# Performance work log

Measured on AMD Instinct MI355X. Metric: run time of the kernel, lower is better.

The kernel has to match this reference:

```python
import jax, jax.numpy as jnp
import numpy as np

D_MODEL = 1024
NUM_HEADS = 16
D_K = D_MODEL // NUM_HEADS
D_FF = 4096
THETA = 10000.0
EPS = 1e-5


def rmsnorm(x, w):
    ms = jnp.mean(jnp.square(x), axis=-1, keepdims=True)
    return x * jax.lax.rsqrt(ms + EPS) * w


def rope(x, pos):
    # x: [B, H, S, d_k]; pos: [S]
    half = x.shape[-1] // 2
    inv_freq = THETA ** (-jnp.arange(half, dtype=x.dtype) * 2.0 / x.shape[-1])  # [half]
    ang = pos.astype(x.dtype)[:, None] * inv_freq[None, :]  # [S, half]
    cos, sin = jnp.cos(ang), jnp.sin(ang)
    xe, xo = x[..., 0::2], x[..., 1::2]
    oe = xe * cos - xo * sin
    oo = xe * sin + xo * cos
    return jnp.stack([oe, oo], axis=-1).reshape(x.shape)


def setup_inputs() -> dict:
    key = jax.random.key(0)
    ks = jax.random.split(key, 10)
    std_d = 1.0 / np.sqrt(D_MODEL)
    std_f = 1.0 / np.sqrt(D_FF)
    B, S = 4, 2048
    return {
        "x": jax.random.normal(ks[0], (B, S, D_MODEL), dtype=jnp.float32),
        "token_positions": jnp.arange(S, dtype=jnp.int32),
        "q_proj": jax.random.normal(ks[1], (D_MODEL, D_MODEL), dtype=jnp.float32) * std_d,
        "k_proj": jax.random.normal(ks[2], (D_MODEL, D_MODEL), dtype=jnp.float32) * std_d,
        "v_proj": jax.random.normal(ks[3], (D_MODEL, D_MODEL), dtype=jnp.float32) * std_d,
        "o_proj": jax.random.normal(ks[4], (D_MODEL, D_MODEL), dtype=jnp.float32) * std_d,
        "w1": jax.random.normal(ks[5], (D_FF, D_MODEL), dtype=jnp.float32) * std_d,
        "w2": jax.random.normal(ks[6], (D_MODEL, D_FF), dtype=jnp.float32) * std_f,
        "w3": jax.random.normal(ks[7], (D_FF, D_MODEL), dtype=jnp.float32) * std_d,
        "ln1_w": jnp.ones((D_MODEL,), dtype=jnp.float32),
        "ln2_w": jnp.ones((D_MODEL,), dtype=jnp.float32),
    }


def reference(x, token_positions, q_proj, k_proj, v_proj, o_proj, w1, w2, w3, ln1_w, ln2_w):
    B, S, _ = x.shape
    x_ln = rmsnorm(x, ln1_w)
    q = x_ln @ q_proj.T
    k = x_ln @ k_proj.T
    v = x_ln @ v_proj.T
    # [B, S, D] -> [B, H, S, d_k]
    def split_heads(t):
        return t.reshape(B, S, NUM_HEADS, D_K).transpose(0, 2, 1, 3)
    q, k, v = split_heads(q), split_heads(k), split_heads(v)
    q = rope(q, token_positions)
    k = rope(k, token_positions)
    scores = jnp.einsum("bhqd,bhkd->bhqk", q, k) / jnp.sqrt(jnp.asarray(D_K, x.dtype))
    causal = jnp.tril(jnp.ones((S, S), dtype=bool))
    scores = jnp.where(causal, scores, -jnp.inf)
    attn = jax.nn.softmax(scores, axis=-1)
    out = jnp.einsum("bhqk,bhkd->bhqd", attn, v)
    out = out.transpose(0, 2, 1, 3).reshape(B, S, D_MODEL)
    x = x + out @ o_proj.T
    x_ln2 = rmsnorm(x, ln2_w)
    u = x_ln2 @ w1.T
    vff = x_ln2 @ w3.T
    ff = (u * jax.nn.sigmoid(u)) * vff
    return x + ff @ w2.T
```

## Files before the change

kernel.cpp:

```cpp
#include <hip/hip_runtime.h>
#include <hip/hip_bf16.h>


typedef unsigned short u16;
typedef __attribute__((ext_vector_type(8))) short short8;
typedef __attribute__((ext_vector_type(4))) float f32x4;
typedef __attribute__((ext_vector_type(16))) float f32x16;

#define MFMA16(a, b, c) __builtin_amdgcn_mfma_f32_16x16x32_bf16(a, b, c, 0, 0, 0)
#define MFMA32(a, b, c) __builtin_amdgcn_mfma_f32_32x32x16_bf16(a, b, c, 0, 0, 0)

__device__ __forceinline__ u16 f2b(float f) {
  union { float f; unsigned u; } x; x.f = f;
  unsigned r = x.u + 0x7FFFu + ((x.u >> 16) & 1u);
  return (u16)(r >> 16);
}
__device__ __forceinline__ float b2f(u16 h) {
  union { unsigned u; float f; } x; x.u = ((unsigned)h) << 16;
  return x.f;
}
__device__ __forceinline__ unsigned pkbf(float a, float b) {
  __hip_bfloat162 h = __float22bfloat162_rn(make_float2(a, b));
  union { __hip_bfloat162 h; unsigned u; } cv; cv.h = h;
  return cv.u;
}
__device__ __forceinline__ void async16(const void* g, void* l) {
  __builtin_amdgcn_global_load_lds(
      (const __attribute__((address_space(1))) void*)g,
      (__attribute__((address_space(3))) void*)l, 16, 0, 0);
}

template <int MODE>
__global__ __launch_bounds__(256, 2) void gemm_bt(
    const u16* __restrict__ A, const u16* __restrict__ B,
    u16* __restrict__ Cb, float* __restrict__ Cf, const float* __restrict__ R,
    int M, int N, int K) {
  __shared__ __align__(16) u16 As[128 * 64];
  __shared__ __align__(16) u16 Bs[128 * 64];
  const int tid = threadIdx.x;
  const int l = tid & 63, w = tid >> 6;
  const int wr = w & 1, wc = w >> 1;
  const int lr = l & 31, lh = l >> 5;
  const size_t m0 = (size_t)blockIdx.y * 128, n0 = (size_t)blockIdx.x * 128;
  f32x16 acc[2][2] = {};
  for (int k0 = 0; k0 < K; k0 += 64) {
#pragma unroll
    for (int t = 0; t < 4; ++t) {
      int c = t * 256 + tid;
      int r = c >> 3;
      int gc = ((c & 7) ^ (r & 7)) << 3;
      async16(A + (m0 + r) * (size_t)K + k0 + gc, &As[c * 8]);
    }
#pragma unroll
    for (int t = 0; t < 4; ++t) {
      int c = t * 256 + tid;
      int r = c >> 3;
      int gc = ((c & 7) ^ (r & 7)) << 3;
      async16(B + (n0 + r) * (size_t)K + k0 + gc, &Bs[c * 8]);
    }
    __syncthreads();
#pragma unroll
    for (int c = 0; c < 4; ++c) {
      const int c8 = c * 2 + lh;
      short8 af[2], bfr[2];
#pragma unroll
      for (int mi = 0; mi < 2; ++mi) {
        int r = wr * 64 + mi * 32 + lr;
        af[mi] = *(const short8*)&As[r * 64 + ((c8 ^ (r & 7)) << 3)];
      }
#pragma unroll
      for (int ni = 0; ni < 2; ++ni) {
        int r = wc * 64 + ni * 32 + lr;
        bfr[ni] = *(const short8*)&Bs[r * 64 + ((c8 ^ (r & 7)) << 3)];
      }
#pragma unroll
      for (int mi = 0; mi < 2; ++mi)
#pragma unroll
        for (int ni = 0; ni < 2; ++ni)
          acc[mi][ni] = MFMA32(af[mi], bfr[ni], acc[mi][ni]);
    }
    __syncthreads();
  }
#pragma unroll
  for (int mi = 0; mi < 2; ++mi)
#pragma unroll
    for (int ni = 0; ni < 2; ++ni) {
      size_t n = n0 + wc * 64 + ni * 32 + lr;
#pragma unroll
      for (int reg = 0; reg < 16; ++reg) {
        size_t m = m0 + wr * 64 + mi * 32 + (reg & 3) + 8 * (reg >> 2) + 4 * lh;
        float v = acc[mi][ni][reg];
        if (MODE == 0)
          Cb[m * (size_t)N + n] = f2b(v);
        else
          Cf[m * (size_t)N + n] = v + R[m * (size_t)N + n];
      }
    }
}

__global__ __launch_bounds__(256, 2) void ffn_gemm(
    const u16* __restrict__ A, const u16* __restrict__ B1,
    const u16* __restrict__ B3, u16* __restrict__ Hout, int M, int N, int K) {
  __shared__ __align__(16) u16 As[128 * 64];
  __shared__ __align__(16) u16 B1s[128 * 64];
  __shared__ __align__(16) u16 B3s[128 * 64];
  const int tid = threadIdx.x;
  const int l = tid & 63, w = tid >> 6;
  const int wr = w & 1, wc = w >> 1;
  const int lr = l & 31, lh = l >> 5;
  const size_t m0 = (size_t)blockIdx.y * 128, n0 = (size_t)blockIdx.x * 128;
  f32x16 a1[2][2] = {}, a3[2][2] = {};
  for (int k0 = 0; k0 < K; k0 += 64) {
#pragma unroll
    for (int t = 0; t < 4; ++t) {
      int c = t * 256 + tid;
      int r = c >> 3;
      int gc = ((c & 7) ^ (r & 7)) << 3;
      async16(A + (m0 + r) * (size_t)K + k0 + gc, &As[c * 8]);
      async16(B1 + (n0 + r) * (size_t)K + k0 + gc, &B1s[c * 8]);
      async16(B3 + (n0 + r) * (size_t)K + k0 + gc, &B3s[c * 8]);
    }
    __syncthreads();
#pragma unroll
    for (int c = 0; c < 4; ++c) {
      const int c8 = c * 2 + lh;
      short8 af[2], b1f[2], b3f[2];
#pragma unroll
      for (int mi = 0; mi < 2; ++mi) {
        int r = wr * 64 + mi * 32 + lr;
        af[mi] = *(const short8*)&As[r * 64 + ((c8 ^ (r & 7)) << 3)];
      }
#pragma unroll
      for (int ni = 0; ni < 2; ++ni) {
        int r = wc * 64 + ni * 32 + lr;
        b1f[ni] = *(const short8*)&B1s[r * 64 + ((c8 ^ (r & 7)) << 3)];
        b3f[ni] = *(const short8*)&B3s[r * 64 + ((c8 ^ (r & 7)) << 3)];
      }
#pragma unroll
      for (int mi = 0; mi < 2; ++mi)
#pragma unroll
        for (int ni = 0; ni < 2; ++ni) {
          a1[mi][ni] = MFMA32(af[mi], b1f[ni], a1[mi][ni]);
          a3[mi][ni] = MFMA32(af[mi], b3f[ni], a3[mi][ni]);
        }
    }
    __syncthreads();
  }
#pragma unroll
  for (int mi = 0; mi < 2; ++mi)
#pragma unroll
    for (int ni = 0; ni < 2; ++ni) {
      size_t n = n0 + wc * 64 + ni * 32 + lr;
#pragma unroll
      for (int reg = 0; reg < 16; ++reg) {
        size_t m = m0 + wr * 64 + mi * 32 + (reg & 3) + 8 * (reg >> 2) + 4 * lh;
        float u = a1[mi][ni][reg];
        float g = u / (1.0f + __expf(-u));
        Hout[m * (size_t)N + n] = f2b(g * a3[mi][ni][reg]);
      }
    }
}

__global__ __launch_bounds__(256, 2) void attn_k(
    const u16* __restrict__ qh, const u16* __restrict__ kh,
    const u16* __restrict__ vt, u16* __restrict__ aout) {
  __shared__ __align__(16) u16 Ks[128 * 64];
  __shared__ __align__(16) u16 Vs[64 * 128];
  __shared__ __align__(16) u16 Ps[64 * 136];
  const int tid = threadIdx.x;
  const int l = tid & 63, w = tid >> 6;
  const int q = l & 15, lq = l >> 4;
  const int q0 = (int)(gridDim.x - 1 - blockIdx.x) * 64;
  const int bh = blockIdx.y;
  const size_t base = (size_t)bh * (2048 * 64);
  const int nt = (q0 + 64 + 127) >> 7;
  const int qcol = q0 + w * 16 + q;

  short8 bq[2];
#pragma unroll
  for (int kk = 0; kk < 2; ++kk)
    bq[kk] = *(const short8*)(qh + base + (size_t)qcol * 64 + kk * 32 + lq * 8);

  f32x4 o[4] = {};
  float mI = -1e30f, lI = 0.0f;

  for (int it = 0; it < nt; ++it) {
    const int kv0 = it << 7;
    if (it) __syncthreads();
#pragma unroll
    for (int t = 0; t < 4; ++t) {
      int p = t * 256 + tid;
      int r = p >> 3, cs = p & 7;
      async16(kh + base + (size_t)(kv0 + r) * 64 + ((cs ^ (r & 7)) << 3), &Ks[p * 8]);
    }
#pragma unroll
    for (int t = 0; t < 4; ++t) {
      int p = t * 256 + tid;
      int r = p >> 4, cs = p & 15;
      async16(vt + base + (size_t)r * 2048 + kv0 + ((cs ^ (r & 15)) << 3), &Vs[p * 8]);
    }
    __syncthreads();
    f32x4 s[8] = {};
#pragma unroll
    for (int kk = 0; kk < 2; ++kk) {
#pragma unroll
      for (int mt = 0; mt < 8; ++mt) {
        int row = mt * 16 + q;
        short8 ak = *(const short8*)&Ks[row * 64 + (((kk * 4 + lq) ^ (q & 7)) << 3)];
        s[mt] = MFMA16(ak, bq[kk], s[mt]);
      }
    }
    if (it == nt - 1) {
#pragma unroll
      for (int mt = 0; mt < 8; ++mt)
#pragma unroll
        for (int r = 0; r < 4; ++r)
          if (kv0 + mt * 16 + lq * 4 + r > qcol) s[mt][r] = -1e30f;
    }
    float mx = -1e30f;
#pragma unroll
    for (int mt = 0; mt < 8; ++mt)
#pragma unroll
      for (int r = 0; r < 4; ++r) mx = fmaxf(mx, s[mt][r]);
    mx = fmaxf(mx, __shfl_xor(mx, 16, 64));
    mx = fmaxf(mx, __shfl_xor(mx, 32, 64));
    const float mn = fmaxf(mI, mx);
    const float al = exp2f(mI - mn);
    mI = mn;
    float rs = 0.0f;
#pragma unroll
    for (int mt = 0; mt < 8; ++mt)
#pragma unroll
      for (int r = 0; r < 4; ++r) {
        float p = exp2f(s[mt][r] - mn);
        s[mt][r] = p;
        rs += p;
      }
    rs += __shfl_xor(rs, 16, 64);
    rs += __shfl_xor(rs, 32, 64);
    lI = lI * al + rs;
#pragma unroll
    for (int mt = 0; mt < 4; ++mt)
#pragma unroll
      for (int r = 0; r < 4; ++r) o[mt][r] *= al;
    u16* pr = &Ps[(w * 16 + q) * 136];
#pragma unroll
    for (int mt = 0; mt < 8; ++mt) {
      uint2 pd;
      pd.x = pkbf(s[mt][0], s[mt][1]);
      pd.y = pkbf(s[mt][2], s[mt][3]);
      *(uint2*)&pr[mt * 16 + lq * 4] = pd;
    }
#pragma unroll
    for (int kk = 0; kk < 4; ++kk) {
      short8 bp = *(const short8*)&pr[kk * 32 + lq * 8];
#pragma unroll
      for (int mt = 0; mt < 4; ++mt) {
        int row = mt * 16 + q;
        short8 av = *(const short8*)&Vs[row * 128 + (((kk * 4 + lq) ^ (row & 15)) << 3)];
        o[mt] = MFMA16(av, bp, o[mt]);
      }
    }
  }
  const int b = bh >> 4, h = bh & 15;
  const float inv = 1.0f / lI;
#pragma unroll
  for (int mt = 0; mt < 4; ++mt) {
    uint2 pd;
    pd.x = pkbf(o[mt][0] * inv, o[mt][1] * inv);
    pd.y = pkbf(o[mt][2] * inv, o[mt][3] * inv);
    *(uint2*)&aout[((size_t)(b * 2048 + qcol)) * 1024 + h * 64 + mt * 16 + lq * 4] = pd;
  }
}

__global__ __launch_bounds__(256) void rmsnorm_k(
    const float* __restrict__ x, const float* __restrict__ w, u16* __restrict__ out) {
  const int row = blockIdx.x;
  const int tid = threadIdx.x;
  const float4 v = ((const float4*)(x + (size_t)row * 1024))[tid];
  float ss = v.x * v.x + v.y * v.y + v.z * v.z + v.w * v.w;
#pragma unroll
  for (int d = 1; d < 64; d <<= 1) ss += __shfl_xor(ss, d, 64);
  __shared__ float red[4];
  if ((tid & 63) == 0) red[tid >> 6] = ss;
  __syncthreads();
  const float sc = rsqrtf((red[0] + red[1] + red[2] + red[3]) * (1.0f / 1024.0f) + 1e-5f);
  const float4 wv = ((const float4*)w)[tid];
  u16* o = out + (size_t)row * 1024 + tid * 4;
  o[0] = f2b(v.x * sc * wv.x);
  o[1] = f2b(v.y * sc * wv.y);
  o[2] = f2b(v.z * sc * wv.z);
  o[3] = f2b(v.w * sc * wv.w);
}

__global__ __launch_bounds__(256) void rope_k(
    const u16* __restrict__ qkv, u16* __restrict__ qh, u16* __restrict__ kh,
    const int* __restrict__ pos) {
  int idx = blockIdx.x * 256 + threadIdx.x;
  int pr = idx & 1023;
  int row = idx >> 10;
  int which = pr >> 9;
  int p = pr & 511;
  int s = row & 2047, b = row >> 11;
  int h = p >> 5, i = p & 31;
  size_t si = (size_t)row * 3072 + which * 1024 + h * 64 + 2 * i;
  float xe = b2f(qkv[si]), xo = b2f(qkv[si + 1]);
  float inv = exp2f(-(float)(2 * i) * (13.287712379549449f / 64.0f));
  float ang = (float)pos[s] * inv;
  float sn, cs;
  __sincosf(ang, &sn, &cs);
  const float scale = which ? 1.0f : 0.18033688011112042f;
  u16* dst = which ? kh : qh;
  size_t od = (((size_t)(b * 16 + h)) * 2048 + s) * 64 + 2 * i;
  dst[od] = f2b((xe * cs - xo * sn) * scale);
  dst[od + 1] = f2b((xe * sn + xo * cs) * scale);
}

__global__ __launch_bounds__(256) void transv_k(
    const u16* __restrict__ qkv, u16* __restrict__ vt) {
  __shared__ u16 t[64][65];
  const int bh = blockIdx.y, s0 = blockIdx.x * 64;
  const int b = bh >> 4, h = bh & 15;
  const int tid = threadIdx.x;
#pragma unroll
  for (int i = 0; i < 16; ++i) {
    int e = i * 256 + tid;
    int sl = e >> 6, d = e & 63;
    t[sl][d] = qkv[((size_t)(b * 2048 + s0 + sl)) * 3072 + 2048 + h * 64 + d];
  }
  __syncthreads();
#pragma unroll
  for (int i = 0; i < 16; ++i) {
    int e = i * 256 + tid;
    int d = e >> 6, sl = e & 63;
    vt[((size_t)(bh * 64 + d)) * 2048 + s0 + sl] = t[sl][d];
  }
}

__global__ __launch_bounds__(256) void cvt_k(
    const float* __restrict__ in, u16* __restrict__ out, int n4) {
  int i = blockIdx.x * 256 + threadIdx.x;
  if (i < n4) {
    float4 v = ((const float4*)in)[i];
    u16* o = out + (size_t)i * 4;
    o[0] = f2b(v.x); o[1] = f2b(v.y); o[2] = f2b(v.z); o[3] = f2b(v.w);
  }
}

extern "C" void kernel_launch(void* const* d_in, const int* in_sizes, int n_in,
                              void* d_out, int out_size, void* d_ws, size_t ws_size,
                              hipStream_t stream) {
  const float* x   = (const float*)d_in[0];
  const int*   pos = (const int*)d_in[1];
  const float* qp  = (const float*)d_in[2];
  const float* kp  = (const float*)d_in[3];
  const float* vp  = (const float*)d_in[4];
  const float* op  = (const float*)d_in[5];
  const float* w1  = (const float*)d_in[6];
  const float* w2  = (const float*)d_in[7];
  const float* w3  = (const float*)d_in[8];
  const float* ln1 = (const float*)d_in[9];
  const float* ln2 = (const float*)d_in[10];
  float* out = (float*)d_out;
  char* ws = (char*)d_ws;
  const size_t MB = 1024 * 1024;

  u16* WQKV = (u16*)(ws + 0 * MB);
  u16* WO   = (u16*)(ws + 6 * MB);
  u16* W1   = (u16*)(ws + 8 * MB);
  u16* W3   = (u16*)(ws + 16 * MB);
  u16* W2   = (u16*)(ws + 24 * MB);
  u16* XLN  = (u16*)(ws + 32 * MB);
  u16* QKV  = (u16*)(ws + 48 * MB);
  u16* QH   = (u16*)(ws + 96 * MB);
  u16* KH   = (u16*)(ws + 112 * MB);
  u16* VT   = (u16*)(ws + 128 * MB);
  u16* ATT  = (u16*)(ws + 48 * MB);
  u16* XLN2 = (u16*)(ws + 64 * MB);
  u16* Hbuf = (u16*)(ws + 80 * MB);
  (void)in_sizes; (void)n_in; (void)out_size; (void)ws_size;

  cvt_k<<<1024, 256, 0, stream>>>(qp, WQKV, 262144);
  cvt_k<<<1024, 256, 0, stream>>>(kp, WQKV + 1024 * 1024, 262144);
  cvt_k<<<1024, 256, 0, stream>>>(vp, WQKV + 2 * 1024 * 1024, 262144);
  cvt_k<<<1024, 256, 0, stream>>>(op, WO, 262144);
  cvt_k<<<4096, 256, 0, stream>>>(w1, W1, 1048576);
  cvt_k<<<4096, 256, 0, stream>>>(w3, W3, 1048576);
  cvt_k<<<4096, 256, 0, stream>>>(w2, W2, 1048576);
  rmsnorm_k<<<8192, 256, 0, stream>>>(x, ln1, XLN);
  gemm_bt<0><<<dim3(24, 64), 256, 0, stream>>>(XLN, WQKV, QKV, nullptr, nullptr, 8192, 3072, 1024);
  rope_k<<<32768, 256, 0, stream>>>(QKV, QH, KH, pos);
  transv_k<<<dim3(32, 64), 256, 0, stream>>>(QKV, VT);
  attn_k<<<dim3(32, 64), 256, 0, stream>>>(QH, KH, VT, ATT);
  gemm_bt<1><<<dim3(8, 64), 256, 0, stream>>>(ATT, WO, nullptr, out, x, 8192, 1024, 1024);
  rmsnorm_k<<<8192, 256, 0, stream>>>(out, ln2, XLN2);
  ffn_gemm<<<dim3(32, 64), 256, 0, stream>>>(XLN2, W1, W3, Hbuf, 8192, 4096, 1024);
  gemm_bt<1><<<dim3(8, 64), 256, 0, stream>>>(Hbuf, W2, nullptr, out, out, 8192, 1024, 4096);
}
```

Measured before the change: 641.4 us.

## Process 128 queries per attention block, vectorize RoPE, merge weight conversions

The attention kernel now handles two 64-query sub-tiles per block, so each K/V tile loaded into shared memory serves 128 queries, halving K/V traffic and the grid size. The RoPE kernel handles 8 elements per thread with 16-byte loads and stores instead of scalar accesses. The seven weight-conversion launches are merged into one kernel to cut launch overhead. The attention change raises register pressure and halves the number of blocks, which can reduce occupancy and load balance on the causal tail.

```diff
diff --git a/kernel.cpp b/kernel.cpp
--- a/kernel.cpp
+++ b/kernel.cpp
@@ -170,19 +170,22 @@
   const int tid = threadIdx.x;
   const int l = tid & 63, w = tid >> 6;
   const int q = l & 15, lq = l >> 4;
-  const int q0 = (int)(gridDim.x - 1 - blockIdx.x) * 64;
+  const int q0 = (int)(gridDim.x - 1 - blockIdx.x) * 128;
   const int bh = blockIdx.y;
   const size_t base = (size_t)bh * (2048 * 64);
-  const int nt = (q0 + 64 + 127) >> 7;
-  const int qcol = q0 + w * 16 + q;
-
-  short8 bq[2];
-#pragma unroll
-  for (int kk = 0; kk < 2; ++kk)
-    bq[kk] = *(const short8*)(qh + base + (size_t)qcol * 64 + kk * 32 + lq * 8);
-
-  f32x4 o[4] = {};
-  float mI = -1e30f, lI = 0.0f;
+  const int nt = (q0 >> 7) + 1;
+
+  int qcol[2] = {q0 + w * 16 + q, q0 + 64 + w * 16 + q};
+  short8 bq[2][2];
+#pragma unroll
+  for (int sub = 0; sub < 2; ++sub)
+#pragma unroll
+    for (int kk = 0; kk < 2; ++kk)
+      bq[sub][kk] = *(const short8*)(qh + base + (size_t)qcol[sub] * 64 + kk * 32 + lq * 8);
+
+  f32x4 o[2][4] = {};
+  float mI[2] = {-1e30f, -1e30f}, lI[2] = {0.0f, 0.0f};
+  u16* pr = &Ps[(w * 16 + q) * 136];
 
   for (int it = 0; it < nt; ++it) {
     const int kv0 = it << 7;
@@ -200,76 +203,82 @@
       async16(vt + base + (size_t)r * 2048 + kv0 + ((cs ^ (r & 15)) << 3), &Vs[p * 8]);
     }
     __syncthreads();
-    f32x4 s[8] = {};
-#pragma unroll
-    for (int kk = 0; kk < 2; ++kk) {
+    const bool last = (it == nt - 1);
+#pragma unroll
+    for (int sub = 0; sub < 2; ++sub) {
+      f32x4 s[8] = {};
+#pragma unroll
+      for (int kk = 0; kk < 2; ++kk) {
+#pragma unroll
+        for (int mt = 0; mt < 8; ++mt) {
+          int row = mt * 16 + q;
+          short8 ak = *(const short8*)&Ks[row * 64 + (((kk * 4 + lq) ^ (q & 7)) << 3)];
+          s[mt] = MFMA16(ak, bq[sub][kk], s[mt]);
+        }
+      }
+      if (last) {
+#pragma unroll
+        for (int mt = 0; mt < 8; ++mt)
+#pragma unroll
+          for (int r = 0; r < 4; ++r)
+            if (kv0 + mt * 16 + lq * 4 + r > qcol[sub]) s[mt][r] = -1e30f;
+      }
+      float mx = -1e30f;
+#pragma unroll
+      for (int mt = 0; mt < 8; ++mt)
+#pragma unroll
+        for (int r = 0; r < 4; ++r) mx = fmaxf(mx, s[mt][r]);
+      mx = fmaxf(mx, __shfl_xor(mx, 16, 64));
+      mx = fmaxf(mx, __shfl_xor(mx, 32, 64));
+      const float mn = fmaxf(mI[sub], mx);
+      const float al = exp2f(mI[sub] - mn);
+      mI[sub] = mn;
+      float rs = 0.0f;
+#pragma unroll
+      for (int mt = 0; mt < 8; ++mt)
+#pragma unroll
+        for (int r = 0; r < 4; ++r) {
+          float p = exp2f(s[mt][r] - mn);
+          s[mt][r] = p;
+          rs += p;
+        }
+      rs += __shfl_xor(rs, 16, 64);
+      rs += __shfl_xor(rs, 32, 64);
+      lI[sub] = lI[sub] * al + rs;
+#pragma unroll
+      for (int mt = 0; mt < 4; ++mt)
+#pragma unroll
+        for (int r = 0; r < 4; ++r) o[sub][mt][r] *= al;
 #pragma unroll
       for (int mt = 0; mt < 8; ++mt) {
-        int row = mt * 16 + q;
-        short8 ak = *(const short8*)&Ks[row * 64 + (((kk * 4 + lq) ^ (q & 7)) << 3)];
-        s[mt] = MFMA16(ak, bq[kk], s[mt]);
-      }
-    }
-    if (it == nt - 1) {
-#pragma unroll
-      for (int mt = 0; mt < 8; ++mt)
-#pragma unroll
-        for (int r = 0; r < 4; ++r)
-          if (kv0 + mt * 16 + lq * 4 + r > qcol) s[mt][r] = -1e30f;
-    }
-    float mx = -1e30f;
-#pragma unroll
-    for (int mt = 0; mt < 8; ++mt)
-#pragma unroll
-      for (int r = 0; r < 4; ++r) mx = fmaxf(mx, s[mt][r]);
-    mx = fmaxf(mx, __shfl_xor(mx, 16, 64));
-    mx = fmaxf(mx, __shfl_xor(mx, 32, 64));
-    const float mn = fmaxf(mI, mx);
-    const float al = exp2f(mI - mn);
-    mI = mn;
-    float rs = 0.0f;
-#pragma unroll
-    for (int mt = 0; mt < 8; ++mt)
-#pragma unroll
-      for (int r = 0; r < 4; ++r) {
-        float p = exp2f(s[mt][r] - mn);
-        s[mt][r] = p;
-        rs += p;
-      }
-    rs += __shfl_xor(rs, 16, 64);
-    rs += __shfl_xor(rs, 32, 64);
-    lI = lI * al + rs;
-#pragma unroll
-    for (int mt = 0; mt < 4; ++mt)
-#pragma unroll
-      for (int r = 0; r < 4; ++r) o[mt][r] *= al;
-    u16* pr = &Ps[(w * 16 + q) * 136];
-#pragma unroll
-    for (int mt = 0; mt < 8; ++mt) {
+        uint2 pd;
+        pd.x = pkbf(s[mt][0], s[mt][1]);
+        pd.y = pkbf(s[mt][2], s[mt][3]);
+        *(uint2*)&pr[mt * 16 + lq * 4] = pd;
+      }
+#pragma unroll
+      for (int kk = 0; kk < 4; ++kk) {
+        short8 bp = *(const short8*)&pr[kk * 32 + lq * 8];
+#pragma unroll
+        for (int mt = 0; mt < 4; ++mt) {
+          int row = mt * 16 + q;
+          short8 av = *(const short8*)&Vs[row * 128 + (((kk * 4 + lq) ^ (row & 15)) << 3)];
+          o[sub][mt] = MFMA16(av, bp, o[sub][mt]);
+        }
+      }
+    }
+  }
+  const int b = bh >> 4, h = bh & 15;
+#pragma unroll
+  for (int sub = 0; sub < 2; ++sub) {
+    const float inv = 1.0f / lI[sub];
+#pragma unroll
+    for (int mt = 0; mt < 4; ++mt) {
       uint2 pd;
-      pd.x = pkbf(s[mt][0], s[mt][1]);
-      pd.y = pkbf(s[mt][2], s[mt][3]);
-      *(uint2*)&pr[mt * 16 + lq * 4] = pd;
-    }
-#pragma unroll
-    for (int kk = 0; kk < 4; ++kk) {
-      short8 bp = *(const short8*)&pr[kk * 32 + lq * 8];
-#pragma unroll
-      for (int mt = 0; mt < 4; ++mt) {
-        int row = mt * 16 + q;
-        short8 av = *(const short8*)&Vs[row * 128 + (((kk * 4 + lq) ^ (row & 15)) << 3)];
-        o[mt] = MFMA16(av, bp, o[mt]);
-      }
-    }
-  }
-  const int b = bh >> 4, h = bh & 15;
-  const float inv = 1.0f / lI;
-#pragma unroll
-  for (int mt = 0; mt < 4; ++mt) {
-    uint2 pd;
-    pd.x = pkbf(o[mt][0] * inv, o[mt][1] * inv);
-    pd.y = pkbf(o[mt][2] * inv, o[mt][3] * inv);
-    *(uint2*)&aout[((size_t)(b * 2048 + qcol)) * 1024 + h * 64 + mt * 16 + lq * 4] = pd;
+      pd.x = pkbf(o[sub][mt][0] * inv, o[sub][mt][1] * inv);
+      pd.y = pkbf(o[sub][mt][2] * inv, o[sub][mt][3] * inv);
+      *(uint2*)&aout[((size_t)(b * 2048 + qcol[sub])) * 1024 + h * 64 + mt * 16 + lq * 4] = pd;
+    }
   }
 }
 
@@ -297,23 +306,31 @@
     const u16* __restrict__ qkv, u16* __restrict__ qh, u16* __restrict__ kh,
     const int* __restrict__ pos) {
   int idx = blockIdx.x * 256 + threadIdx.x;
-  int pr = idx & 1023;
-  int row = idx >> 10;
-  int which = pr >> 9;
-  int p = pr & 511;
+  int grp = idx & 255;
+  int row = idx >> 8;
+  int which = grp >> 7;
+  int p = grp & 127;
   int s = row & 2047, b = row >> 11;
-  int h = p >> 5, i = p & 31;
-  size_t si = (size_t)row * 3072 + which * 1024 + h * 64 + 2 * i;
-  float xe = b2f(qkv[si]), xo = b2f(qkv[si + 1]);
-  float inv = exp2f(-(float)(2 * i) * (13.287712379549449f / 64.0f));
-  float ang = (float)pos[s] * inv;
-  float sn, cs;
-  __sincosf(ang, &sn, &cs);
+  int h = p >> 3, gi = p & 7;
+  const u16* src = qkv + (size_t)row * 3072 + which * 1024 + h * 64 + gi * 8;
+  uint4 in = *(const uint4*)src;
+  const u16* e = (const u16*)&in;
+  const float fp = (float)pos[s];
   const float scale = which ? 1.0f : 0.18033688011112042f;
-  u16* dst = which ? kh : qh;
-  size_t od = (((size_t)(b * 16 + h)) * 2048 + s) * 64 + 2 * i;
-  dst[od] = f2b((xe * cs - xo * sn) * scale);
-  dst[od + 1] = f2b((xe * sn + xo * cs) * scale);
+  uint4 outv;
+  unsigned* ov = (unsigned*)&outv;
+#pragma unroll
+  for (int j = 0; j < 4; ++j) {
+    int i = gi * 4 + j;
+    float xe = b2f(e[2 * j]), xo = b2f(e[2 * j + 1]);
+    float inv = exp2f(-(float)(2 * i) * (13.287712379549449f / 64.0f));
+    float ang = fp * inv;
+    float sn, cs;
+    __sincosf(ang, &sn, &cs);
+    ov[j] = pkbf((xe * cs - xo * sn) * scale, (xe * sn + xo * cs) * scale);
+  }
+  u16* dst = (which ? kh : qh) + (((size_t)(b * 16 + h)) * 2048 + s) * 64 + gi * 8;
+  *(uint4*)dst = outv;
 }
 
 __global__ __launch_bounds__(256) void transv_k(
@@ -337,14 +354,32 @@
   }
 }
 
-__global__ __launch_bounds__(256) void cvt_k(
-    const float* __restrict__ in, u16* __restrict__ out, int n4) {
+__global__ __launch_bounds__(256) void cvt_all(
+    const float* __restrict__ qp, const float* __restrict__ kp,
+    const float* __restrict__ vp, const float* __restrict__ op,
+    const float* __restrict__ w1, const float* __restrict__ w3,
+    const float* __restrict__ w2,
+    u16* __restrict__ WQKV, u16* __restrict__ WO,
+    u16* __restrict__ W1, u16* __restrict__ W3, u16* __restrict__ W2) {
   int i = blockIdx.x * 256 + threadIdx.x;
-  if (i < n4) {
-    float4 v = ((const float4*)in)[i];
-    u16* o = out + (size_t)i * 4;
-    o[0] = f2b(v.x); o[1] = f2b(v.y); o[2] = f2b(v.z); o[3] = f2b(v.w);
-  }
+  const float* src;
+  u16* dst;
+  int off;
+  if (i < 1048576) {
+    int seg = i >> 18, within = i & 262143;
+    src = (seg == 0) ? qp : (seg == 1) ? kp : (seg == 2) ? vp : op;
+    dst = (seg == 3) ? WO : WQKV + (size_t)seg * 1048576;
+    off = within;
+  } else {
+    int j = i - 1048576;
+    int seg = j >> 20;
+    off = j & 1048575;
+    src = (seg == 0) ? w1 : (seg == 1) ? w3 : w2;
+    dst = (seg == 0) ? W1 : (seg == 1) ? W3 : W2;
+  }
+  float4 v = ((const float4*)src)[off];
+  u16* o = dst + (size_t)off * 4;
+  o[0] = f2b(v.x); o[1] = f2b(v.y); o[2] = f2b(v.z); o[3] = f2b(v.w);
 }
 
 extern "C" void kernel_launch(void* const* d_in, const int* in_sizes, int n_in,
@@ -380,18 +415,13 @@
   u16* Hbuf = (u16*)(ws + 80 * MB);
   (void)in_sizes; (void)n_in; (void)out_size; (void)ws_size;
 
-  cvt_k<<<1024, 256, 0, stream>>>(qp, WQKV, 262144);
-  cvt_k<<<1024, 256, 0, stream>>>(kp, WQKV + 1024 * 1024, 262144);
-  cvt_k<<<1024, 256, 0, stream>>>(vp, WQKV + 2 * 1024 * 1024, 262144);
-  cvt_k<<<1024, 256, 0, stream>>>(op, WO, 262144);
-  cvt_k<<<4096, 256, 0, stream>>>(w1, W1, 1048576);
-  cvt_k<<<4096, 256, 0, stream>>>(w3, W3, 1048576);
-  cvt_k<<<4096, 256, 0, stream>>>(w2, W2, 1048576);
+  cvt_all<<<16384, 256, 0, stream>>>(qp, kp, vp, op, w1, w3, w2,
+                                     WQKV, WO, W1, W3, W2);
   rmsnorm_k<<<8192, 256, 0, stream>>>(x, ln1, XLN);
   gemm_bt<0><<<dim3(24, 64), 256, 0, stream>>>(XLN, WQKV, QKV, nullptr, nullptr, 8192, 3072, 1024);
-  rope_k<<<32768, 256, 0, stream>>>(QKV, QH, KH, pos);
+  rope_k<<<8192, 256, 0, stream>>>(QKV, QH, KH, pos);
   transv_k<<<dim3(32, 64), 256, 0, stream>>>(QKV, VT);
-  attn_k<<<dim3(32, 64), 256, 0, stream>>>(QH, KH, VT, ATT);
+  attn_k<<<dim3(16, 64), 256, 0, stream>>>(QH, KH, VT, ATT);
   gemm_bt<1><<<dim3(8, 64), 256, 0, stream>>>(ATT, WO, nullptr, out, x, 8192, 1024, 1024);
   rmsnorm_k<<<8192, 256, 0, stream>>>(out, ln2, XLN2);
   ffn_gemm<<<dim3(32, 64), 256, 0, stream>>>(XLN2, W1, W3, Hbuf, 8192, 4096, 1024);
```

After: 629.1 us. Within noise of the previous version (-1.9%).
